# Kernel optimization log

Measured on AMD Instinct MI355X. Metric: run time of the kernel, lower is better.

The kernel has to match this reference:

```python
import jax, jax.numpy as jnp
import numpy as np

BS = 8  # DCT block size


def _dct_basis():
    x = np.arange(BS)
    u = np.arange(BS)
    M = 0.5 * np.cos((2 * x[None, :] + 1) * u[:, None] * np.pi / 16)
    M[0, :] *= 1.0 / np.sqrt(2.0)
    # Separable 2-D basis: coeff[u, v, x, y] = M[u, x] * M[v, y]
    return jnp.asarray(np.einsum('ux,vy->uvxy', M, M), jnp.float32)


_Q_LUM = np.array([
    [16, 11, 10, 16, 24, 40, 51, 61],
    [12, 12, 14, 19, 26, 58, 60, 55],
    [14, 13, 16, 24, 40, 57, 69, 56],
    [14, 17, 22, 29, 51, 87, 80, 62],
    [18, 22, 37, 56, 68, 109, 103, 77],
    [24, 35, 55, 64, 81, 104, 113, 92],
    [49, 64, 78, 87, 103, 121, 120, 101],
    [72, 92, 95, 98, 112, 100, 103, 99]], dtype=np.float32)

_Q_CHROM = np.array([
    [17, 18, 24, 47, 99, 99, 99, 99],
    [18, 21, 26, 66, 99, 99, 99, 99],
    [24, 26, 56, 99, 99, 99, 99, 99],
    [47, 66, 99, 99, 99, 99, 99, 99],
    [99, 99, 99, 99, 99, 99, 99, 99],
    [99, 99, 99, 99, 99, 99, 99, 99],
    [99, 99, 99, 99, 99, 99, 99, 99],
    [99, 99, 99, 99, 99, 99, 99, 99]], dtype=np.float32)


def setup_inputs() -> dict:
    key = jax.random.key(0)
    image = jax.random.uniform(key, (16, 3, 512, 512), dtype=jnp.float32)
    rgb2yuv = jnp.array([[0.299, 0.587, 0.114],
                         [-0.1687, -0.3313, 0.5],
                         [0.5, -0.4187, -0.0813]], jnp.float32)
    yuv2rgb = jnp.array([[1.0, 0.0, 1.402],
                         [1.0, -0.34414, -0.71414],
                         [1.0, 1.772, 0.0]], jnp.float32)
    return {
        'image': image,
        'rgb2yuv': rgb2yuv,
        'yuv2rgb': yuv2rgb,
        'dct_coeff': _dct_basis(),          # (8,8,8,8)
        'q_lum': jnp.asarray(_Q_LUM),       # (8,8)
        'q_chrom': jnp.asarray(_Q_CHROM),   # (8,8)
    }


def _compress(x, C, Q):
    # x: (b, c, H, W) with H, W multiples of 8; C: (8,8,8,8); Q: (8,8)
    b, c, H, W = x.shape
    nh, nw = H // BS, W // BS
    x = x * 255.0 - 128.0
    # tile into 8x8 blocks: (b, c, nh, nw, 8, 8)
    blk = x.reshape(b, c, nh, BS, nw, BS).transpose(0, 1, 2, 4, 3, 5)
    # forward block DCT: out[u,v] = sum_{x,y} C[u,v,x,y] * blk[x,y]
    d = jnp.einsum('uvxy,bcnmxy->bcnmuv', C, blk)
    # quantize / dequantize (Q broadcasts over the last two (u, v) dims)
    d = jnp.round(d / Q) * Q
    # inverse block DCT (transpose of the orthonormal basis)
    r = jnp.einsum('xyuv,bcnmuv->bcnmxy', C, d)
    img = r.transpose(0, 1, 2, 4, 3, 5).reshape(b, c, H, W)
    return (img + 128.0) / 255.0


def reference(image, rgb2yuv, yuv2rgb, dct_coeff, q_lum, q_chrom):
    yuv = jnp.einsum('ij,bjhw->bihw', rgb2yuv, image)
    y = _compress(yuv[:, 0:1], dct_coeff, q_lum)
    uv = _compress(yuv[:, 1:], dct_coeff, q_chrom)
    out = jnp.einsum('ij,bjhw->bihw', yuv2rgb, jnp.concatenate([y, uv], axis=1))
    return out
```

## Files before the change

kernel.cpp:

```cpp
#include <hip/hip_runtime.h>
#include <math.h>

#define CSTRIDE (512 * 512)

__device__ __forceinline__ float chain_dot64_nofma(const float* __restrict__ c,
                                                   const float* __restrict__ v)
{
#pragma clang fp contract(off)
    float s = 0.0f;
#pragma unroll
    for (int q = 0; q < 64; ++q) s = s + c[q] * v[q];
    return s;
}

__global__ __launch_bounds__(256)
void jpeg_kernel(const float* __restrict__ img,
                 const float* __restrict__ rgb2yuv,
                 const float* __restrict__ yuv2rgb,
                 const float* __restrict__ dctC,
                 const float* __restrict__ qlum,
                 const float* __restrict__ qchrom,
                 float* __restrict__ out)
{
#pragma clang fp contract(off)
    __shared__ float A[4096];
    __shared__ float B[4096];

    const int tid  = threadIdx.x;
    const int lane = tid & 63;
    const int wv   = tid >> 6;
    const int p0u  = __builtin_amdgcn_readfirstlane(wv * 16);

    const int b  = blockIdx.x >> 6;
    const int y0 = (blockIdx.x & 63) << 3;
    const size_t base0 = (size_t)b * 3 * CSTRIDE + (size_t)y0 * 512;

    const float r00 = rgb2yuv[0], r01 = rgb2yuv[1], r02 = rgb2yuv[2];
    const float r10 = rgb2yuv[3], r11 = rgb2yuv[4], r12 = rgb2yuv[5];
    const float r20 = rgb2yuv[6], r21 = rgb2yuv[7], r22 = rgb2yuv[8];

#pragma unroll
    for (int i = 0; i < 4; ++i) {
        const size_t f4 = 4 * (size_t)(tid + 256 * i);
        const float4 R4 = *(const float4*)(img + base0 + f4);
        const float4 G4 = *(const float4*)(img + base0 + CSTRIDE + f4);
        const float4 B4 = *(const float4*)(img + base0 + 2 * CSTRIDE + f4);
        const float* rp = (const float*)&R4;
        const float* gp = (const float*)&G4;
        const float* bp = (const float*)&B4;
#pragma unroll
        for (int jj = 0; jj < 4; ++jj) {
            const int flat = 4 * (tid + 256 * i) + jj;
            const int w = flat & 511, x = flat >> 9;
            const int idx = ((x << 3) + (w & 7)) * 64 + (w >> 3);
            const float r_ = rp[jj], g_ = gp[jj], b_ = bp[jj];
            float t;
            t = (r00 * r_ + r01 * g_) + r02 * b_;  A[idx] = t * 255.0f - 128.0f;
            t = (r10 * r_ + r11 * g_) + r12 * b_;  B[idx] = t * 255.0f - 128.0f;
        }
    }
    __syncthreads();

    const int xb = __builtin_amdgcn_readfirstlane(wv * 2);
    float mrow[2][8];
#pragma unroll
    for (int k = 0; k < 2; ++k)
#pragma unroll
        for (int u = 0; u < 8; ++u)
            mrow[k][u] = dctC[(size_t)(xb + k) * 512 + u * 8] * 2.82842712474619f;

    const float MT[8][8] = {
        { 0.353553391f,  0.353553391f,  0.353553391f,  0.353553391f,  0.353553391f,  0.353553391f,  0.353553391f,  0.353553391f},
        { 0.490392640f,  0.415734806f,  0.277785117f,  0.097545161f, -0.097545161f, -0.277785117f, -0.415734806f, -0.490392640f},
        { 0.461939766f,  0.191341716f, -0.191341716f, -0.461939766f, -0.461939766f, -0.191341716f,  0.191341716f,  0.461939766f},
        { 0.415734806f, -0.097545161f, -0.490392640f, -0.277785117f,  0.277785117f,  0.490392640f,  0.097545161f, -0.415734806f},
        { 0.353553391f, -0.353553391f, -0.353553391f,  0.353553391f,  0.353553391f, -0.353553391f, -0.353553391f,  0.353553391f},
        { 0.277785117f, -0.490392640f,  0.097545161f,  0.415734806f, -0.415734806f, -0.097545161f,  0.490392640f, -0.277785117f},
        { 0.191341716f, -0.461939766f,  0.461939766f, -0.191341716f, -0.191341716f,  0.461939766f, -0.461939766f,  0.191341716f},
        { 0.097545161f, -0.277785117f,  0.415734806f, -0.490392640f,  0.490392640f, -0.415734806f,  0.277785117f, -0.097545161f}};

    auto proc = [&](float* Vc, const float* qtab) {
        float v[64];
#pragma unroll
        for (int q = 0; q < 64; ++q) v[q] = Vc[q * 64 + lane];
        __syncthreads();

        for (int j = 0; j < 16; ++j) {
            const float* Crow = dctC + (size_t)(p0u + j) * 64;
            const float d  = chain_dot64_nofma(Crow, v);
            const float qv = qtab[p0u + j];
            const float dq = rintf(d / qv) * qv;
            Vc[(p0u + j) * 64 + lane] = dq;
        }
        __syncthreads();

        float t[64];
#pragma unroll
        for (int u = 0; u < 8; ++u) {
            float du[8];
#pragma unroll
            for (int q = 0; q < 8; ++q) du[q] = Vc[(u * 8 + q) * 64 + lane];
#pragma unroll
            for (int y = 0; y < 8; ++y) {
                float s = MT[y][0] * du[0];
#pragma unroll
                for (int q = 1; q < 8; ++q) s = fmaf(MT[y][q], du[q], s);
                t[u * 8 + y] = s;
            }
        }
        __syncthreads();

#pragma unroll
        for (int j = 0; j < 16; ++j) {
            const int k = j >> 3, y = j & 7;
            float s = mrow[k][0] * t[y];
#pragma unroll
            for (int u = 1; u < 8; ++u) s = fmaf(mrow[k][u], t[u * 8 + y], s);
            Vc[(p0u + j) * 64 + lane] = s;
        }
    };

    proc(A, qlum);
    __syncthreads();

    float recY[16];
#pragma unroll
    for (int i = 0; i < 4; ++i) {
#pragma unroll
        for (int jj = 0; jj < 4; ++jj) {
            const int flat = 4 * (tid + 256 * i) + jj;
            const int w = flat & 511, x = flat >> 9;
            recY[i * 4 + jj] = A[((x << 3) + (w & 7)) * 64 + (w >> 3)];
        }
    }
    __syncthreads();

#pragma unroll
    for (int i = 0; i < 4; ++i) {
        const size_t f4 = 4 * (size_t)(tid + 256 * i);
        const float4 R4 = *(const float4*)(img + base0 + f4);
        const float4 G4 = *(const float4*)(img + base0 + CSTRIDE + f4);
        const float4 B4 = *(const float4*)(img + base0 + 2 * CSTRIDE + f4);
        const float* rp = (const float*)&R4;
        const float* gp = (const float*)&G4;
        const float* bp = (const float*)&B4;
#pragma unroll
        for (int jj = 0; jj < 4; ++jj) {
            const int flat = 4 * (tid + 256 * i) + jj;
            const int w = flat & 511, x = flat >> 9;
            const int idx = ((x << 3) + (w & 7)) * 64 + (w >> 3);
            const float tW = (r20 * rp[jj] + r21 * gp[jj]) + r22 * bp[jj];
            A[idx] = tW * 255.0f - 128.0f;
        }
    }
    __syncthreads();

    proc(A, qchrom);
    proc(B, qchrom);
    __syncthreads();

    const float s255 = 1.0f / 255.0f;
    const float c00 = yuv2rgb[0] * s255, c01 = yuv2rgb[1] * s255, c02 = yuv2rgb[2] * s255;
    const float c10 = yuv2rgb[3] * s255, c11 = yuv2rgb[4] * s255, c12 = yuv2rgb[5] * s255;
    const float c20 = yuv2rgb[6] * s255, c21 = yuv2rgb[7] * s255, c22 = yuv2rgb[8] * s255;
    const float k0 = (yuv2rgb[0] + yuv2rgb[1] + yuv2rgb[2]) * (128.0f / 255.0f);
    const float k1 = (yuv2rgb[3] + yuv2rgb[4] + yuv2rgb[5]) * (128.0f / 255.0f);
    const float k2 = (yuv2rgb[6] + yuv2rgb[7] + yuv2rgb[8]) * (128.0f / 255.0f);

#pragma unroll
    for (int i = 0; i < 4; ++i) {
        float4 o0, o1, o2;
        float* q0 = (float*)&o0; float* q1 = (float*)&o1; float* q2 = (float*)&o2;
#pragma unroll
        for (int jj = 0; jj < 4; ++jj) {
            const int flat = 4 * (tid + 256 * i) + jj;
            const int w = flat & 511, x = flat >> 9;
            const int cell = ((x << 3) + (w & 7)) * 64 + (w >> 3);
            const float Yv = recY[i * 4 + jj];
            const float Uv = B[cell];
            const float Wv = A[cell];
            q0[jj] = fmaf(c00, Yv, fmaf(c01, Uv, fmaf(c02, Wv, k0)));
            q1[jj] = fmaf(c10, Yv, fmaf(c11, Uv, fmaf(c12, Wv, k1)));
            q2[jj] = fmaf(c20, Yv, fmaf(c21, Uv, fmaf(c22, Wv, k2)));
        }
        const size_t f4 = 4 * (size_t)(tid + 256 * i);
        *(float4*)(out + base0 + f4)                = o0;
        *(float4*)(out + base0 + CSTRIDE + f4)      = o1;
        *(float4*)(out + base0 + 2 * CSTRIDE + f4)  = o2;
    }
}

extern "C" void kernel_launch(void* const* d_in, const int* in_sizes, int n_in,
                              void* d_out, int out_size, void* d_ws, size_t ws_size,
                              hipStream_t stream) {
    const float* img = (const float*)d_in[0];
    const float* r2y = (const float*)d_in[1];
    const float* y2r = (const float*)d_in[2];
    const float* C   = (const float*)d_in[3];
    const float* ql  = (const float*)d_in[4];
    const float* qc  = (const float*)d_in[5];
    float* o = (float*)d_out;

    jpeg_kernel<<<dim3(16 * 64), dim3(256), 0, stream>>>(img, r2y, y2r, C, ql, qc, o);
}
```

Baseline: 166.1 us.

## Use packed FP32 math for forward DCT and hold all three channels in LDS

Adds a small init kernel that interleaves pairs of DCT basis rows into a workspace buffer. The main kernel then computes the forward DCT two output coefficients at a time with v_pk_mul_f32/v_pk_add_f32 inline asm, which halves the VALU instruction count of the dominant 64-term dot products while keeping the non-FMA rounding order. All three YUV channels are now kept in a 48KB LDS array, so the image is read only once instead of being reloaded for the W channel. Launch bounds request 3 blocks per CU. The extra LDS and register pressure may limit occupancy, and the path depends on a workspace being available, with a scalar fallback otherwise.

```diff
diff --git a/kernel.cpp b/kernel.cpp
--- a/kernel.cpp
+++ b/kernel.cpp
@@ -2,6 +2,8 @@
 #include <math.h>
 
 #define CSTRIDE (512 * 512)
+
+typedef float v2f __attribute__((ext_vector_type(2)));
 
 __device__ __forceinline__ float chain_dot64_nofma(const float* __restrict__ c,
                                                    const float* __restrict__ v)
@@ -13,23 +15,35 @@
     return s;
 }
 
-__global__ __launch_bounds__(256)
-void jpeg_kernel(const float* __restrict__ img,
-                 const float* __restrict__ rgb2yuv,
-                 const float* __restrict__ yuv2rgb,
-                 const float* __restrict__ dctC,
-                 const float* __restrict__ qlum,
-                 const float* __restrict__ qchrom,
-                 float* __restrict__ out)
+__global__ void init_pc(const float* __restrict__ dctC, v2f* __restrict__ pc)
+{
+    const int idx = blockIdx.x * 256 + threadIdx.x;
+    const int jp = idx >> 6, q = idx & 63;
+    const int w = jp >> 3, j = jp & 7;
+    v2f c;
+    c.x = dctC[(size_t)(16 * w + j) * 64 + q];
+    c.y = dctC[(size_t)(16 * w + j + 8) * 64 + q];
+    pc[idx] = c;
+}
+
+__global__ __launch_bounds__(256, 3)
+void jpeg_kernel_pk(const float* __restrict__ img,
+                    const float* __restrict__ rgb2yuv,
+                    const float* __restrict__ yuv2rgb,
+                    const float* __restrict__ dctC,
+                    const float* __restrict__ qlum,
+                    const float* __restrict__ qchrom,
+                    float* __restrict__ out,
+                    const v2f* __restrict__ pc)
 {
 #pragma clang fp contract(off)
-    __shared__ float A[4096];
-    __shared__ float B[4096];
+    __shared__ float V[3][4096];
 
     const int tid  = threadIdx.x;
     const int lane = tid & 63;
     const int wv   = tid >> 6;
     const int p0u  = __builtin_amdgcn_readfirstlane(wv * 16);
+    const int jb   = __builtin_amdgcn_readfirstlane(wv * 8);
 
     const int b  = blockIdx.x >> 6;
     const int y0 = (blockIdx.x & 63) << 3;
@@ -55,8 +69,9 @@
             const int idx = ((x << 3) + (w & 7)) * 64 + (w >> 3);
             const float r_ = rp[jj], g_ = gp[jj], b_ = bp[jj];
             float t;
-            t = (r00 * r_ + r01 * g_) + r02 * b_;  A[idx] = t * 255.0f - 128.0f;
-            t = (r10 * r_ + r11 * g_) + r12 * b_;  B[idx] = t * 255.0f - 128.0f;
+            t = (r00 * r_ + r01 * g_) + r02 * b_;  V[0][idx] = t * 255.0f - 128.0f;
+            t = (r10 * r_ + r11 * g_) + r12 * b_;  V[1][idx] = t * 255.0f - 128.0f;
+            t = (r20 * r_ + r21 * g_) + r22 * b_;  V[2][idx] = t * 255.0f - 128.0f;
         }
     }
     __syncthreads();
@@ -79,18 +94,42 @@
         { 0.191341716f, -0.461939766f,  0.461939766f, -0.191341716f, -0.191341716f,  0.461939766f, -0.461939766f,  0.191341716f},
         { 0.097545161f, -0.277785117f,  0.415734806f, -0.490392640f,  0.490392640f, -0.415734806f,  0.277785117f, -0.097545161f}};
 
-    auto proc = [&](float* Vc, const float* qtab) {
-        float v[64];
-#pragma unroll
-        for (int q = 0; q < 64; ++q) v[q] = Vc[q * 64 + lane];
-        __syncthreads();
-
-        for (int j = 0; j < 16; ++j) {
-            const float* Crow = dctC + (size_t)(p0u + j) * 64;
-            const float d  = chain_dot64_nofma(Crow, v);
-            const float qv = qtab[p0u + j];
-            const float dq = rintf(d / qv) * qv;
-            Vc[(p0u + j) * 64 + lane] = dq;
+    for (int c = 0; c < 3; ++c) {
+        float* Vc = V[c];
+
+        v2f v2[32];
+#pragma unroll
+        for (int qq = 0; qq < 32; ++qq) {
+            v2f t;
+            t.x = Vc[(2 * qq) * 64 + lane];
+            t.y = Vc[(2 * qq + 1) * 64 + lane];
+            v2[qq] = t;
+        }
+        __syncthreads();
+
+        const float* qtab = (c == 0) ? qlum : qchrom;
+        for (int j = 0; j < 8; ++j) {
+            const v2f* crow = pc + (size_t)(jb + j) * 64;
+            v2f acc; acc.x = 0.0f; acc.y = 0.0f;
+#pragma unroll
+            for (int q = 0; q < 64; ++q) {
+                const v2f c2 = crow[q];
+                v2f p2;
+                if ((q & 1) == 0)
+                    asm("v_pk_mul_f32 %0, %1, %2 op_sel:[0,0] op_sel_hi:[1,0]"
+                        : "=v"(p2) : "s"(c2), "v"(v2[q >> 1]));
+                else
+                    asm("v_pk_mul_f32 %0, %1, %2 op_sel:[0,1] op_sel_hi:[1,1]"
+                        : "=v"(p2) : "s"(c2), "v"(v2[q >> 1]));
+                asm("v_pk_add_f32 %0, %0, %1 op_sel:[0,0] op_sel_hi:[1,1]"
+                    : "+v"(acc) : "v"(p2));
+            }
+            const float qA = qtab[p0u + j];
+            const float qB = qtab[p0u + j + 8];
+            const float dqA = rintf(acc.x / qA) * qA;
+            const float dqB = rintf(acc.y / qB) * qB;
+            Vc[(p0u + j) * 64 + lane]     = dqA;
+            Vc[(p0u + j + 8) * 64 + lane] = dqB;
         }
         __syncthreads();
 
@@ -118,22 +157,62 @@
             for (int u = 1; u < 8; ++u) s = fmaf(mrow[k][u], t[u * 8 + y], s);
             Vc[(p0u + j) * 64 + lane] = s;
         }
-    };
-
-    proc(A, qlum);
+    }
     __syncthreads();
 
-    float recY[16];
+    const float s255 = 1.0f / 255.0f;
+    const float c00 = yuv2rgb[0] * s255, c01 = yuv2rgb[1] * s255, c02 = yuv2rgb[2] * s255;
+    const float c10 = yuv2rgb[3] * s255, c11 = yuv2rgb[4] * s255, c12 = yuv2rgb[5] * s255;
+    const float c20 = yuv2rgb[6] * s255, c21 = yuv2rgb[7] * s255, c22 = yuv2rgb[8] * s255;
+    const float k0 = (yuv2rgb[0] + yuv2rgb[1] + yuv2rgb[2]) * (128.0f / 255.0f);
+    const float k1 = (yuv2rgb[3] + yuv2rgb[4] + yuv2rgb[5]) * (128.0f / 255.0f);
+    const float k2 = (yuv2rgb[6] + yuv2rgb[7] + yuv2rgb[8]) * (128.0f / 255.0f);
+
 #pragma unroll
     for (int i = 0; i < 4; ++i) {
+        float4 o0, o1, o2;
+        float* q0 = (float*)&o0; float* q1 = (float*)&o1; float* q2 = (float*)&o2;
 #pragma unroll
         for (int jj = 0; jj < 4; ++jj) {
             const int flat = 4 * (tid + 256 * i) + jj;
             const int w = flat & 511, x = flat >> 9;
-            recY[i * 4 + jj] = A[((x << 3) + (w & 7)) * 64 + (w >> 3)];
-        }
-    }
-    __syncthreads();
+            const int cell = ((x << 3) + (w & 7)) * 64 + (w >> 3);
+            const float Yv = V[0][cell], Uv = V[1][cell], Wv = V[2][cell];
+            q0[jj] = fmaf(c00, Yv, fmaf(c01, Uv, fmaf(c02, Wv, k0)));
+            q1[jj] = fmaf(c10, Yv, fmaf(c11, Uv, fmaf(c12, Wv, k1)));
+            q2[jj] = fmaf(c20, Yv, fmaf(c21, Uv, fmaf(c22, Wv, k2)));
+        }
+        const size_t f4 = 4 * (size_t)(tid + 256 * i);
+        *(float4*)(out + base0 + f4)                = o0;
+        *(float4*)(out + base0 + CSTRIDE + f4)      = o1;
+        *(float4*)(out + base0 + 2 * CSTRIDE + f4)  = o2;
+    }
+}
+
+__global__ __launch_bounds__(256, 3)
+void jpeg_kernel_sc(const float* __restrict__ img,
+                    const float* __restrict__ rgb2yuv,
+                    const float* __restrict__ yuv2rgb,
+                    const float* __restrict__ dctC,
+                    const float* __restrict__ qlum,
+                    const float* __restrict__ qchrom,
+                    float* __restrict__ out)
+{
+#pragma clang fp contract(off)
+    __shared__ float V[3][4096];
+
+    const int tid  = threadIdx.x;
+    const int lane = tid & 63;
+    const int wv   = tid >> 6;
+    const int p0u  = __builtin_amdgcn_readfirstlane(wv * 16);
+
+    const int b  = blockIdx.x >> 6;
+    const int y0 = (blockIdx.x & 63) << 3;
+    const size_t base0 = (size_t)b * 3 * CSTRIDE + (size_t)y0 * 512;
+
+    const float r00 = rgb2yuv[0], r01 = rgb2yuv[1], r02 = rgb2yuv[2];
+    const float r10 = rgb2yuv[3], r11 = rgb2yuv[4], r12 = rgb2yuv[5];
+    const float r20 = rgb2yuv[6], r21 = rgb2yuv[7], r22 = rgb2yuv[8];
 
 #pragma unroll
     for (int i = 0; i < 4; ++i) {
@@ -149,14 +228,75 @@
             const int flat = 4 * (tid + 256 * i) + jj;
             const int w = flat & 511, x = flat >> 9;
             const int idx = ((x << 3) + (w & 7)) * 64 + (w >> 3);
-            const float tW = (r20 * rp[jj] + r21 * gp[jj]) + r22 * bp[jj];
-            A[idx] = tW * 255.0f - 128.0f;
+            const float r_ = rp[jj], g_ = gp[jj], b_ = bp[jj];
+            float t;
+            t = (r00 * r_ + r01 * g_) + r02 * b_;  V[0][idx] = t * 255.0f - 128.0f;
+            t = (r10 * r_ + r11 * g_) + r12 * b_;  V[1][idx] = t * 255.0f - 128.0f;
+            t = (r20 * r_ + r21 * g_) + r22 * b_;  V[2][idx] = t * 255.0f - 128.0f;
         }
     }
     __syncthreads();
 
-    proc(A, qchrom);
-    proc(B, qchrom);
+    const int xb = __builtin_amdgcn_readfirstlane(wv * 2);
+    float mrow[2][8];
+#pragma unroll
+    for (int k = 0; k < 2; ++k)
+#pragma unroll
+        for (int u = 0; u < 8; ++u)
+            mrow[k][u] = dctC[(size_t)(xb + k) * 512 + u * 8] * 2.82842712474619f;
+
+    const float MT[8][8] = {
+        { 0.353553391f,  0.353553391f,  0.353553391f,  0.353553391f,  0.353553391f,  0.353553391f,  0.353553391f,  0.353553391f},
+        { 0.490392640f,  0.415734806f,  0.277785117f,  0.097545161f, -0.097545161f, -0.277785117f, -0.415734806f, -0.490392640f},
+        { 0.461939766f,  0.191341716f, -0.191341716f, -0.461939766f, -0.461939766f, -0.191341716f,  0.191341716f,  0.461939766f},
+        { 0.415734806f, -0.097545161f, -0.490392640f, -0.277785117f,  0.277785117f,  0.490392640f,  0.097545161f, -0.415734806f},
+        { 0.353553391f, -0.353553391f, -0.353553391f,  0.353553391f,  0.353553391f, -0.353553391f, -0.353553391f,  0.353553391f},
+        { 0.277785117f, -0.490392640f,  0.097545161f,  0.415734806f, -0.415734806f, -0.097545161f,  0.490392640f, -0.277785117f},
+        { 0.191341716f, -0.461939766f,  0.461939766f, -0.191341716f, -0.191341716f,  0.461939766f, -0.461939766f,  0.191341716f},
+        { 0.097545161f, -0.277785117f,  0.415734806f, -0.490392640f,  0.490392640f, -0.415734806f,  0.277785117f, -0.097545161f}};
+
+    for (int c = 0; c < 3; ++c) {
+        float* Vc = V[c];
+        float v[64];
+#pragma unroll
+        for (int q = 0; q < 64; ++q) v[q] = Vc[q * 64 + lane];
+        __syncthreads();
+
+        const float* qtab = (c == 0) ? qlum : qchrom;
+        for (int j = 0; j < 16; ++j) {
+            const float* Crow = dctC + (size_t)(p0u + j) * 64;
+            const float d  = chain_dot64_nofma(Crow, v);
+            const float qv = qtab[p0u + j];
+            const float dq = rintf(d / qv) * qv;
+            Vc[(p0u + j) * 64 + lane] = dq;
+        }
+        __syncthreads();
+
+        float t[64];
+#pragma unroll
+        for (int u = 0; u < 8; ++u) {
+            float du[8];
+#pragma unroll
+            for (int q = 0; q < 8; ++q) du[q] = Vc[(u * 8 + q) * 64 + lane];
+#pragma unroll
+            for (int y = 0; y < 8; ++y) {
+                float s = MT[y][0] * du[0];
+#pragma unroll
+                for (int q = 1; q < 8; ++q) s = fmaf(MT[y][q], du[q], s);
+                t[u * 8 + y] = s;
+            }
+        }
+        __syncthreads();
+
+#pragma unroll
+        for (int j = 0; j < 16; ++j) {
+            const int k = j >> 3, y = j & 7;
+            float s = mrow[k][0] * t[y];
+#pragma unroll
+            for (int u = 1; u < 8; ++u) s = fmaf(mrow[k][u], t[u * 8 + y], s);
+            Vc[(p0u + j) * 64 + lane] = s;
+        }
+    }
     __syncthreads();
 
     const float s255 = 1.0f / 255.0f;
@@ -176,9 +316,7 @@
             const int flat = 4 * (tid + 256 * i) + jj;
             const int w = flat & 511, x = flat >> 9;
             const int cell = ((x << 3) + (w & 7)) * 64 + (w >> 3);
-            const float Yv = recY[i * 4 + jj];
-            const float Uv = B[cell];
-            const float Wv = A[cell];
+            const float Yv = V[0][cell], Uv = V[1][cell], Wv = V[2][cell];
             q0[jj] = fmaf(c00, Yv, fmaf(c01, Uv, fmaf(c02, Wv, k0)));
             q1[jj] = fmaf(c10, Yv, fmaf(c11, Uv, fmaf(c12, Wv, k1)));
             q2[jj] = fmaf(c20, Yv, fmaf(c21, Uv, fmaf(c22, Wv, k2)));
@@ -201,5 +339,11 @@
     const float* qc  = (const float*)d_in[5];
     float* o = (float*)d_out;
 
-    jpeg_kernel<<<dim3(16 * 64), dim3(256), 0, stream>>>(img, r2y, y2r, C, ql, qc, o);
-}
+    if (ws_size >= 2048 * sizeof(v2f)) {
+        v2f* pc = (v2f*)d_ws;
+        init_pc<<<dim3(8), dim3(256), 0, stream>>>(C, pc);
+        jpeg_kernel_pk<<<dim3(16 * 64), dim3(256), 0, stream>>>(img, r2y, y2r, C, ql, qc, o, pc);
+    } else {
+        jpeg_kernel_sc<<<dim3(16 * 64), dim3(256), 0, stream>>>(img, r2y, y2r, C, ql, qc, o);
+    }
+}
```

After: 168.5 us. Within noise of the previous version (+1.4%).
